# Optimization experiments

Hardware: AMD Instinct MI355X
Metric: run time of the kernel (lower is better)

Reference implementation:

```python
import jax, jax.numpy as jnp
import numpy as np

VOCAB = 32000
EMBED = 256
HIDDEN = 512
BATCH = 32
MAXLEN = 128


def setup_inputs() -> dict:
    key = jax.random.key(0)
    ks = jax.random.split(key, 8)
    s = 0.02
    return {
        "text": jax.random.randint(ks[0], (BATCH, MAXLEN), 0, VOCAB, dtype=jnp.int64),
        "embed": jax.random.normal(ks[1], (VOCAB, EMBED), dtype=jnp.float32) * s,
        "W_ih": jax.random.normal(ks[2], (4 * HIDDEN, EMBED), dtype=jnp.float32) * s,
        "W_hh": jax.random.normal(ks[3], (4 * HIDDEN, HIDDEN), dtype=jnp.float32) * s,
        "b_ih": jax.random.normal(ks[4], (4 * HIDDEN,), dtype=jnp.float32) * s,
        "b_hh": jax.random.normal(ks[5], (4 * HIDDEN,), dtype=jnp.float32) * s,
        "W_fc": jax.random.normal(ks[6], (VOCAB, HIDDEN), dtype=jnp.float32) * s,
        "b_fc": jax.random.normal(ks[7], (VOCAB,), dtype=jnp.float32) * s,
    }


def reference(text, embed, W_ih, W_hh, b_ih, b_hh, W_fc, b_fc):
    B, T = text.shape
    H = W_hh.shape[1]

    def step(carry, _):
        h, c, tok = carry
        x = embed[tok]                                  # [B, E] gather
        gates = x @ W_ih.T + b_ih + h @ W_hh.T + b_hh   # [B, 4H]
        i, f, g, o = jnp.split(gates, 4, axis=-1)       # PyTorch LSTMCell gate order
        i = jax.nn.sigmoid(i)
        f = jax.nn.sigmoid(f)
        g = jnp.tanh(g)
        o = jax.nn.sigmoid(o)
        c = f * c + i * g
        h = o * jnp.tanh(c)
        logits = h @ W_fc.T + b_fc                      # [B, V]
        tok = jnp.argmax(logits, axis=1)                # greedy feedback
        return (h, c, tok), logits

    # initial prediction = zeros[B,1] -> argmax = token 0; hidden=None -> zeros
    init = (
        jnp.zeros((B, H), dtype=embed.dtype),
        jnp.zeros((B, H), dtype=embed.dtype),
        jnp.zeros((B,), dtype=jnp.int32),
    )
    _, logits = jax.lax.scan(step, init, None, length=T)  # [T, B, V]
    return jnp.transpose(logits, (1, 0, 2))               # [B, T, V]
```

## Files before the change

kernel.cpp:

```cpp
#include <hip/hip_runtime.h>
#include <hip/hip_bf16.h>
#include <math.h>

#define VOCAB  32000
#define EMBED  256
#define HIDDEN 512
#define BATCH  32
#define MAXLEN 128
#define NCAND  250
#define VB     128

typedef __attribute__((ext_vector_type(8))) short bf16x8;
typedef __attribute__((ext_vector_type(8))) unsigned short ushort8;
typedef __attribute__((ext_vector_type(4))) float f32x4;

#define WS_C_OFF     0
#define WS_HHI_OFF   65536
#define WS_HLO_OFF   131072
#define WS_CAND_OFF  196608
#define WS_WHI_OFF   260608
#define WS_WLO_OFF   33028608
#define WS_ZERO_BYTES 196608

__device__ __forceinline__ unsigned int f32_ordered_key(float f) {
    unsigned int b = __float_as_uint(f);
    return (b & 0x80000000u) ? ~b : (b | 0x80000000u);
}
__device__ __forceinline__ unsigned short f2bf(float x) {
    __hip_bfloat16 h = __float2bfloat16(x);
    return *reinterpret_cast<unsigned short*>(&h);
}
__device__ __forceinline__ float bf2f(unsigned short u) {
    __hip_bfloat16 h = *reinterpret_cast<__hip_bfloat16*>(&u);
    return __bfloat162float(h);
}

__global__ __launch_bounds__(256) void split_w_kernel(
    const float* __restrict__ W, unsigned short* __restrict__ hi,
    unsigned short* __restrict__ lo, int n4)
{
    const int stride = gridDim.x * blockDim.x;
    for (int i = blockIdx.x * blockDim.x + threadIdx.x; i < n4; i += stride) {
        f32x4 w = ((const f32x4*)W)[i];
        ushort4 hv, lv;
        #pragma unroll
        for (int j = 0; j < 4; ++j) {
            float x = w[j];
            unsigned short hb = f2bf(x);
            ((unsigned short*)&hv)[j] = hb;
            ((unsigned short*)&lv)[j] = f2bf(x - bf2f(hb));
        }
        ((ushort4*)hi)[i] = hv;
        ((ushort4*)lo)[i] = lv;
    }
}

__global__ __launch_bounds__(256) void lstm_step_kernel(
    const float* __restrict__ embed,
    const float* __restrict__ W_ih, const float* __restrict__ W_hh,
    const float* __restrict__ b_ih, const float* __restrict__ b_hh,
    const unsigned long long* __restrict__ cand,
    const unsigned short* __restrict__ hhi_prev, const unsigned short* __restrict__ hlo_prev,
    unsigned short* __restrict__ hhi_next, unsigned short* __restrict__ hlo_next,
    float* __restrict__ c_buf, int t)
{
    __shared__ float x_t[EMBED][33];
    __shared__ float h_t[HIDDEN][33];
    __shared__ int   tok_s[BATCH];
    __shared__ unsigned long long credl[8][BATCH];
    __shared__ float part[2][4][BATCH][4];
    __shared__ float gate_s[2][4][BATCH];

    const int tid = threadIdx.x;

    if (t > 0) {
        const int rb = tid & 31, seg = tid >> 5;
        unsigned long long m = 0ull;
        for (int i = seg; i < NCAND; i += 8) {
            unsigned long long e = cand[(size_t)i * BATCH + rb];
            if (e > m) m = e;
        }
        credl[seg][rb] = m;
        __syncthreads();
        if (tid < BATCH) {
            unsigned long long mm = credl[0][tid];
            #pragma unroll
            for (int ss = 1; ss < 8; ++ss) if (credl[ss][tid] > mm) mm = credl[ss][tid];
            tok_s[tid] = (int)(~(unsigned int)(mm & 0xFFFFFFFFull));
        }
    } else {
        if (tid < BATCH) tok_s[tid] = 0;
    }
    __syncthreads();

    {
        const int sb = tid >> 3, slot = tid & 7;
        const float* er = embed + (size_t)tok_s[sb] * EMBED;
        #pragma unroll
        for (int i = 0; i < 8; ++i) {
            int e4 = i * 8 + slot;
            float4 v = ((const float4*)er)[e4];
            int e = e4 * 4;
            x_t[e + 0][sb] = v.x; x_t[e + 1][sb] = v.y;
            x_t[e + 2][sb] = v.z; x_t[e + 3][sb] = v.w;
        }
        const ushort8* hr = (const ushort8*)(hhi_prev + (size_t)sb * HIDDEN);
        const ushort8* lr = (const ushort8*)(hlo_prev + (size_t)sb * HIDDEN);
        #pragma unroll
        for (int i = 0; i < 8; ++i) {
            int u = i * 8 + slot;
            ushort8 hv = hr[u], lv = lr[u];
            #pragma unroll
            for (int e = 0; e < 8; ++e)
                h_t[u * 8 + e][sb] = bf2f((unsigned short)hv[e]) + bf2f((unsigned short)lv[e]);
        }
    }
    __syncthreads();

    const int b  = tid & 31;
    const int s  = (tid >> 5) & 3;
    const int jp = tid >> 7;
    const int j  = blockIdx.x * 2 + jp;

    float a0 = 0.f, a1 = 0.f, a2 = 0.f, a3 = 0.f;
    float d0 = 0.f, d1 = 0.f, d2 = 0.f, d3 = 0.f;

    {
        const float4* w0 = (const float4*)(W_ih + (size_t)j * EMBED) + s * 16;
        const float4* w1 = (const float4*)(W_ih + (size_t)(HIDDEN + j) * EMBED) + s * 16;
        const float4* w2 = (const float4*)(W_ih + (size_t)(2 * HIDDEN + j) * EMBED) + s * 16;
        const float4* w3 = (const float4*)(W_ih + (size_t)(3 * HIDDEN + j) * EMBED) + s * 16;
        #pragma unroll 4
        for (int g = 0; g < 16; ++g) {
            float4 W0 = w0[g], W1 = w1[g], W2 = w2[g], W3 = w3[g];
            int e = s * 64 + g * 4;
            float x0 = x_t[e + 0][b], x1 = x_t[e + 1][b], x2 = x_t[e + 2][b], x3 = x_t[e + 3][b];
            a0 = fmaf(W0.x, x0, a0); d0 = fmaf(W0.y, x1, d0); a0 = fmaf(W0.z, x2, a0); d0 = fmaf(W0.w, x3, d0);
            a1 = fmaf(W1.x, x0, a1); d1 = fmaf(W1.y, x1, d1); a1 = fmaf(W1.z, x2, a1); d1 = fmaf(W1.w, x3, d1);
            a2 = fmaf(W2.x, x0, a2); d2 = fmaf(W2.y, x1, d2); a2 = fmaf(W2.z, x2, a2); d2 = fmaf(W2.w, x3, d2);
            a3 = fmaf(W3.x, x0, a3); d3 = fmaf(W3.y, x1, d3); a3 = fmaf(W3.z, x2, a3); d3 = fmaf(W3.w, x3, d3);
        }
    }
    {
        const float4* w0 = (const float4*)(W_hh + (size_t)j * HIDDEN) + s * 32;
        const float4* w1 = (const float4*)(W_hh + (size_t)(HIDDEN + j) * HIDDEN) + s * 32;
        const float4* w2 = (const float4*)(W_hh + (size_t)(2 * HIDDEN + j) * HIDDEN) + s * 32;
        const float4* w3 = (const float4*)(W_hh + (size_t)(3 * HIDDEN + j) * HIDDEN) + s * 32;
        #pragma unroll 4
        for (int g = 0; g < 32; ++g) {
            float4 W0 = w0[g], W1 = w1[g], W2 = w2[g], W3 = w3[g];
            int k = s * 128 + g * 4;
            float x0 = h_t[k + 0][b], x1 = h_t[k + 1][b], x2 = h_t[k + 2][b], x3 = h_t[k + 3][b];
            a0 = fmaf(W0.x, x0, a0); d0 = fmaf(W0.y, x1, d0); a0 = fmaf(W0.z, x2, a0); d0 = fmaf(W0.w, x3, d0);
            a1 = fmaf(W1.x, x0, a1); d1 = fmaf(W1.y, x1, d1); a1 = fmaf(W1.z, x2, a1); d1 = fmaf(W1.w, x3, d1);
            a2 = fmaf(W2.x, x0, a2); d2 = fmaf(W2.y, x1, d2); a2 = fmaf(W2.z, x2, a2); d2 = fmaf(W2.w, x3, d2);
            a3 = fmaf(W3.x, x0, a3); d3 = fmaf(W3.y, x1, d3); a3 = fmaf(W3.z, x2, a3); d3 = fmaf(W3.w, x3, d3);
        }
    }
    part[jp][s][b][0] = a0 + d0;
    part[jp][s][b][1] = a1 + d1;
    part[jp][s][b][2] = a2 + d2;
    part[jp][s][b][3] = a3 + d3;
    __syncthreads();

    {
        const int gb = tid & 31, gate = (tid >> 5) & 3, gjp = tid >> 7;
        const int jj = blockIdx.x * 2 + gjp;
        float g = part[gjp][0][gb][gate] + part[gjp][1][gb][gate]
                + part[gjp][2][gb][gate] + part[gjp][3][gb][gate];
        g += b_ih[gate * HIDDEN + jj] + b_hh[gate * HIDDEN + jj];
        gate_s[gjp][gate][gb] = (gate == 2) ? tanhf(g) : 1.f / (1.f + expf(-g));
    }
    __syncthreads();

    if (tid < 64) {
        const int cb = tid & 31, cjp = tid >> 5;
        const int jj = blockIdx.x * 2 + cjp;
        const float iv = gate_s[cjp][0][cb], fv = gate_s[cjp][1][cb];
        const float gv = gate_s[cjp][2][cb], ov = gate_s[cjp][3][cb];
        const size_t off = (size_t)cb * HIDDEN + jj;
        float cn = fv * c_buf[off] + iv * gv;
        c_buf[off] = cn;
        float hv = ov * tanhf(cn);
        unsigned short hh = f2bf(hv);
        hhi_next[off] = hh;
        hlo_next[off] = f2bf(hv - bf2f(hh));
    }
}

#define MFMA(a, b, c) __builtin_amdgcn_mfma_f32_16x16x32_bf16((a), (b), (c), 0, 0, 0)
#define HPTR(arr, bb, cc) \
    ((const bf16x8*)((const char*)(arr) + ((((bb) * 1024) + (kg * 16) + (cc) * 64) ^ ((((bb) & 7)) << 4))))

__global__ __launch_bounds__(512) void logits_mfma_kernel(
    const unsigned short* __restrict__ Whi, const unsigned short* __restrict__ Wlo,
    const unsigned short* __restrict__ hhi, const unsigned short* __restrict__ hlo,
    const float* __restrict__ b_fc, float* __restrict__ out,
    unsigned long long* __restrict__ cand, int t)
{
    __shared__ unsigned short hs_hi[BATCH * HIDDEN];
    __shared__ unsigned short hs_lo[BATCH * HIDDEN];
    __shared__ unsigned long long red[8][BATCH];

    const int tid = threadIdx.x;

    const int w    = tid >> 6;
    const int lane = tid & 63;
    const int row  = lane & 15;
    const int kg   = lane >> 4;
    const int vwave = blockIdx.x * VB + w * 16;

    const unsigned short* wh = Whi + (size_t)(vwave + row) * HIDDEN + kg * 8;
    const unsigned short* wl = Wlo + (size_t)(vwave + row) * HIDDEN + kg * 8;

    bf16x8 whb[8], wlb[8];
    #pragma unroll
    for (int p = 0; p < 8; ++p) {
        whb[p] = *(const bf16x8*)(wh + p * 32);
        wlb[p] = *(const bf16x8*)(wl + p * 32);
    }

    #pragma unroll
    for (int i = 0; i < 8; ++i) {
        int u   = i * 512 + tid;
        int arr = u >> 11;
        int b   = (u >> 6) & 31;
        int k16 = u & 63;
        const unsigned short* src = (arr ? hlo : hhi) + (size_t)b * HIDDEN + k16 * 8;
        int4 v = *(const int4*)src;
        char* dst = (char*)(arr ? hs_lo : hs_hi) + ((b * 1024 + k16 * 16) ^ ((b & 7) << 4));
        *(int4*)dst = v;
    }
    __syncthreads();

    f32x4 acc0 = {0.f, 0.f, 0.f, 0.f};
    f32x4 acc1 = {0.f, 0.f, 0.f, 0.f};

    #pragma unroll
    for (int c = 0; c < 16; ++c) {
        bf16x8 cwh = whb[c & 7], cwl = wlb[c & 7];
        bf16x8 hh0 = *HPTR(hs_hi, row, c),      hh1 = *HPTR(hs_hi, row + 16, c);
        bf16x8 hl0 = *HPTR(hs_lo, row, c),      hl1 = *HPTR(hs_lo, row + 16, c);
        if (c + 8 < 16) {
            whb[c & 7] = *(const bf16x8*)(wh + (c + 8) * 32);
            wlb[c & 7] = *(const bf16x8*)(wl + (c + 8) * 32);
        }
        acc0 = MFMA(cwh, hh0, acc0); acc1 = MFMA(cwh, hh1, acc1);
        acc0 = MFMA(cwl, hh0, acc0); acc1 = MFMA(cwl, hh1, acc1);
        acc0 = MFMA(cwh, hl0, acc0); acc1 = MFMA(cwh, hl1, acc1);
    }

    const int v4 = vwave + kg * 4;
    f32x4 bias = *(const f32x4*)(b_fc + v4);
    f32x4 st0, st1;
    unsigned long long best0 = 0ull, best1 = 0ull;
    #pragma unroll
    for (int jj = 0; jj < 4; ++jj) {
        st0[jj] = acc0[jj] + bias[jj];
        st1[jj] = acc1[jj] + bias[jj];
        unsigned long long e0 = ((unsigned long long)f32_ordered_key(st0[jj]) << 32)
                              | (unsigned long long)(~(unsigned int)(v4 + jj));
        unsigned long long e1 = ((unsigned long long)f32_ordered_key(st1[jj]) << 32)
                              | (unsigned long long)(~(unsigned int)(v4 + jj));
        if (e0 > best0) best0 = e0;
        if (e1 > best1) best1 = e1;
    }
    __builtin_nontemporal_store(st0, (f32x4*)(out + ((size_t)row * MAXLEN + t) * VOCAB + v4));
    __builtin_nontemporal_store(st1, (f32x4*)(out + ((size_t)(row + 16) * MAXLEN + t) * VOCAB + v4));

    #pragma unroll
    for (int sft = 16; sft <= 32; sft <<= 1) {
        unsigned long long o0 = __shfl_xor(best0, sft, 64);
        unsigned long long o1 = __shfl_xor(best1, sft, 64);
        if (o0 > best0) best0 = o0;
        if (o1 > best1) best1 = o1;
    }
    if (kg == 0) { red[w][row] = best0; red[w][row + 16] = best1; }
    __syncthreads();
    if (tid < BATCH) {
        unsigned long long m = red[0][tid];
        #pragma unroll
        for (int ww = 1; ww < 8; ++ww) if (red[ww][tid] > m) m = red[ww][tid];
        cand[(size_t)blockIdx.x * BATCH + tid] = m;
    }
}

extern "C" void kernel_launch(void* const* d_in, const int* in_sizes, int n_in,
                              void* d_out, int out_size, void* d_ws, size_t ws_size,
                              hipStream_t stream) {
    const float* embed = (const float*)d_in[1];
    const float* W_ih  = (const float*)d_in[2];
    const float* W_hh  = (const float*)d_in[3];
    const float* b_ih  = (const float*)d_in[4];
    const float* b_hh  = (const float*)d_in[5];
    const float* W_fc  = (const float*)d_in[6];
    const float* b_fc  = (const float*)d_in[7];
    float* out = (float*)d_out;

    char* ws = (char*)d_ws;
    float* c_buf = (float*)(ws + WS_C_OFF);
    unsigned short* h_hi = (unsigned short*)(ws + WS_HHI_OFF);
    unsigned short* h_lo = (unsigned short*)(ws + WS_HLO_OFF);
    unsigned long long* cand = (unsigned long long*)(ws + WS_CAND_OFF);
    unsigned short* W_hi = (unsigned short*)(ws + WS_WHI_OFF);
    unsigned short* W_lo = (unsigned short*)(ws + WS_WLO_OFF);

    hipMemsetAsync(d_ws, 0, WS_ZERO_BYTES, stream);
    split_w_kernel<<<2048, 256, 0, stream>>>(W_fc, W_hi, W_lo, VOCAB * HIDDEN / 4);

    for (int t = 0; t < MAXLEN; ++t) {
        const int p = t & 1;
        unsigned short* hhi_prev = h_hi + (size_t)p * BATCH * HIDDEN;
        unsigned short* hlo_prev = h_lo + (size_t)p * BATCH * HIDDEN;
        unsigned short* hhi_next = h_hi + (size_t)(p ^ 1) * BATCH * HIDDEN;
        unsigned short* hlo_next = h_lo + (size_t)(p ^ 1) * BATCH * HIDDEN;
        lstm_step_kernel<<<256, 256, 0, stream>>>(
            embed, W_ih, W_hh, b_ih, b_hh, cand,
            hhi_prev, hlo_prev, hhi_next, hlo_next, c_buf, t);
        logits_mfma_kernel<<<NCAND, 512, 0, stream>>>(
            W_hi, W_lo, hhi_next, hlo_next, b_fc, out, cand, t);
    }
}
```

Baseline: 4.478 ms.

## Drop LDS staging in LSTM step; one hidden unit per block, 512 blocks

The LSTM step kernel no longer stages the embedding rows and hidden state into transposed shared-memory tiles. Each thread now reads its batch row's x and h slices straight from global memory into registers. Each block handles one hidden unit instead of two, with the K dimension split across 8 segments, and the grid doubles to 512 blocks. This removes the LDS fill, one barrier and per-block staging latency, and adds parallelism, at the cost of redundant global reads of x/h across blocks and uncoalesced per-thread row access.

```diff
diff --git a/kernel.cpp b/kernel.cpp
--- a/kernel.cpp
+++ b/kernel.cpp
@@ -64,14 +64,13 @@
     unsigned short* __restrict__ hhi_next, unsigned short* __restrict__ hlo_next,
     float* __restrict__ c_buf, int t)
 {
-    __shared__ float x_t[EMBED][33];
-    __shared__ float h_t[HIDDEN][33];
     __shared__ int   tok_s[BATCH];
     __shared__ unsigned long long credl[8][BATCH];
-    __shared__ float part[2][4][BATCH][4];
-    __shared__ float gate_s[2][4][BATCH];
+    __shared__ float part[8][4][BATCH];
+    __shared__ float gate_s[4][BATCH];
 
     const int tid = threadIdx.x;
+    const int j   = blockIdx.x;
 
     if (t > 0) {
         const int rb = tid & 31, seg = tid >> 5;
@@ -93,92 +92,74 @@
     }
     __syncthreads();
 
+    const int b = tid & 31;
+    const int s = tid >> 5;
+
+    float a0 = 0.f, a1 = 0.f, a2 = 0.f, a3 = 0.f;
+    float d0 = 0.f, d1 = 0.f, d2 = 0.f, d3 = 0.f;
+
     {
-        const int sb = tid >> 3, slot = tid & 7;
-        const float* er = embed + (size_t)tok_s[sb] * EMBED;
+        const float4* xr = (const float4*)(embed + (size_t)tok_s[b] * EMBED + s * 32);
+        const float4* w0 = (const float4*)(W_ih + (size_t)j * EMBED) + s * 8;
+        const float4* w1 = (const float4*)(W_ih + (size_t)(HIDDEN + j) * EMBED) + s * 8;
+        const float4* w2 = (const float4*)(W_ih + (size_t)(2 * HIDDEN + j) * EMBED) + s * 8;
+        const float4* w3 = (const float4*)(W_ih + (size_t)(3 * HIDDEN + j) * EMBED) + s * 8;
+        #pragma unroll
+        for (int g = 0; g < 8; ++g) {
+            float4 xv = xr[g];
+            float4 W0 = w0[g], W1 = w1[g], W2 = w2[g], W3 = w3[g];
+            a0 = fmaf(W0.x, xv.x, a0); d0 = fmaf(W0.y, xv.y, d0); a0 = fmaf(W0.z, xv.z, a0); d0 = fmaf(W0.w, xv.w, d0);
+            a1 = fmaf(W1.x, xv.x, a1); d1 = fmaf(W1.y, xv.y, d1); a1 = fmaf(W1.z, xv.z, a1); d1 = fmaf(W1.w, xv.w, d1);
+            a2 = fmaf(W2.x, xv.x, a2); d2 = fmaf(W2.y, xv.y, d2); a2 = fmaf(W2.z, xv.z, a2); d2 = fmaf(W2.w, xv.w, d2);
+            a3 = fmaf(W3.x, xv.x, a3); d3 = fmaf(W3.y, xv.y, d3); a3 = fmaf(W3.z, xv.z, a3); d3 = fmaf(W3.w, xv.w, d3);
+        }
+    }
+    {
+        const ushort8* hr = (const ushort8*)(hhi_prev + (size_t)b * HIDDEN + s * 64);
+        const ushort8* lr = (const ushort8*)(hlo_prev + (size_t)b * HIDDEN + s * 64);
+        const float4* w0 = (const float4*)(W_hh + (size_t)j * HIDDEN) + s * 16;
+        const float4* w1 = (const float4*)(W_hh + (size_t)(HIDDEN + j) * HIDDEN) + s * 16;
+        const float4* w2 = (const float4*)(W_hh + (size_t)(2 * HIDDEN + j) * HIDDEN) + s * 16;
+        const float4* w3 = (const float4*)(W_hh + (size_t)(3 * HIDDEN + j) * HIDDEN) + s * 16;
         #pragma unroll
         for (int i = 0; i < 8; ++i) {
-            int e4 = i * 8 + slot;
-            float4 v = ((const float4*)er)[e4];
-            int e = e4 * 4;
-            x_t[e + 0][sb] = v.x; x_t[e + 1][sb] = v.y;
-            x_t[e + 2][sb] = v.z; x_t[e + 3][sb] = v.w;
-        }
-        const ushort8* hr = (const ushort8*)(hhi_prev + (size_t)sb * HIDDEN);
-        const ushort8* lr = (const ushort8*)(hlo_prev + (size_t)sb * HIDDEN);
-        #pragma unroll
-        for (int i = 0; i < 8; ++i) {
-            int u = i * 8 + slot;
-            ushort8 hv = hr[u], lv = lr[u];
+            ushort8 hv = hr[i], lv = lr[i];
+            float hf[8];
             #pragma unroll
             for (int e = 0; e < 8; ++e)
-                h_t[u * 8 + e][sb] = bf2f((unsigned short)hv[e]) + bf2f((unsigned short)lv[e]);
-        }
-    }
-    __syncthreads();
-
-    const int b  = tid & 31;
-    const int s  = (tid >> 5) & 3;
-    const int jp = tid >> 7;
-    const int j  = blockIdx.x * 2 + jp;
-
-    float a0 = 0.f, a1 = 0.f, a2 = 0.f, a3 = 0.f;
-    float d0 = 0.f, d1 = 0.f, d2 = 0.f, d3 = 0.f;
-
-    {
-        const float4* w0 = (const float4*)(W_ih + (size_t)j * EMBED) + s * 16;
-        const float4* w1 = (const float4*)(W_ih + (size_t)(HIDDEN + j) * EMBED) + s * 16;
-        const float4* w2 = (const float4*)(W_ih + (size_t)(2 * HIDDEN + j) * EMBED) + s * 16;
-        const float4* w3 = (const float4*)(W_ih + (size_t)(3 * HIDDEN + j) * EMBED) + s * 16;
-        #pragma unroll 4
-        for (int g = 0; g < 16; ++g) {
-            float4 W0 = w0[g], W1 = w1[g], W2 = w2[g], W3 = w3[g];
-            int e = s * 64 + g * 4;
-            float x0 = x_t[e + 0][b], x1 = x_t[e + 1][b], x2 = x_t[e + 2][b], x3 = x_t[e + 3][b];
-            a0 = fmaf(W0.x, x0, a0); d0 = fmaf(W0.y, x1, d0); a0 = fmaf(W0.z, x2, a0); d0 = fmaf(W0.w, x3, d0);
-            a1 = fmaf(W1.x, x0, a1); d1 = fmaf(W1.y, x1, d1); a1 = fmaf(W1.z, x2, a1); d1 = fmaf(W1.w, x3, d1);
-            a2 = fmaf(W2.x, x0, a2); d2 = fmaf(W2.y, x1, d2); a2 = fmaf(W2.z, x2, a2); d2 = fmaf(W2.w, x3, d2);
-            a3 = fmaf(W3.x, x0, a3); d3 = fmaf(W3.y, x1, d3); a3 = fmaf(W3.z, x2, a3); d3 = fmaf(W3.w, x3, d3);
-        }
-    }
-    {
-        const float4* w0 = (const float4*)(W_hh + (size_t)j * HIDDEN) + s * 32;
-        const float4* w1 = (const float4*)(W_hh + (size_t)(HIDDEN + j) * HIDDEN) + s * 32;
-        const float4* w2 = (const float4*)(W_hh + (size_t)(2 * HIDDEN + j) * HIDDEN) + s * 32;
-        const float4* w3 = (const float4*)(W_hh + (size_t)(3 * HIDDEN + j) * HIDDEN) + s * 32;
-        #pragma unroll 4
-        for (int g = 0; g < 32; ++g) {
-            float4 W0 = w0[g], W1 = w1[g], W2 = w2[g], W3 = w3[g];
-            int k = s * 128 + g * 4;
-            float x0 = h_t[k + 0][b], x1 = h_t[k + 1][b], x2 = h_t[k + 2][b], x3 = h_t[k + 3][b];
-            a0 = fmaf(W0.x, x0, a0); d0 = fmaf(W0.y, x1, d0); a0 = fmaf(W0.z, x2, a0); d0 = fmaf(W0.w, x3, d0);
-            a1 = fmaf(W1.x, x0, a1); d1 = fmaf(W1.y, x1, d1); a1 = fmaf(W1.z, x2, a1); d1 = fmaf(W1.w, x3, d1);
-            a2 = fmaf(W2.x, x0, a2); d2 = fmaf(W2.y, x1, d2); a2 = fmaf(W2.z, x2, a2); d2 = fmaf(W2.w, x3, d2);
-            a3 = fmaf(W3.x, x0, a3); d3 = fmaf(W3.y, x1, d3); a3 = fmaf(W3.z, x2, a3); d3 = fmaf(W3.w, x3, d3);
-        }
-    }
-    part[jp][s][b][0] = a0 + d0;
-    part[jp][s][b][1] = a1 + d1;
-    part[jp][s][b][2] = a2 + d2;
-    part[jp][s][b][3] = a3 + d3;
-    __syncthreads();
-
-    {
-        const int gb = tid & 31, gate = (tid >> 5) & 3, gjp = tid >> 7;
-        const int jj = blockIdx.x * 2 + gjp;
-        float g = part[gjp][0][gb][gate] + part[gjp][1][gb][gate]
-                + part[gjp][2][gb][gate] + part[gjp][3][gb][gate];
-        g += b_ih[gate * HIDDEN + jj] + b_hh[gate * HIDDEN + jj];
-        gate_s[gjp][gate][gb] = (gate == 2) ? tanhf(g) : 1.f / (1.f + expf(-g));
-    }
-    __syncthreads();
-
-    if (tid < 64) {
-        const int cb = tid & 31, cjp = tid >> 5;
-        const int jj = blockIdx.x * 2 + cjp;
-        const float iv = gate_s[cjp][0][cb], fv = gate_s[cjp][1][cb];
-        const float gv = gate_s[cjp][2][cb], ov = gate_s[cjp][3][cb];
-        const size_t off = (size_t)cb * HIDDEN + jj;
+                hf[e] = bf2f((unsigned short)hv[e]) + bf2f((unsigned short)lv[e]);
+            #pragma unroll
+            for (int q = 0; q < 2; ++q) {
+                float4 W0 = w0[i * 2 + q], W1 = w1[i * 2 + q], W2 = w2[i * 2 + q], W3 = w3[i * 2 + q];
+                float x0 = hf[q * 4 + 0], x1 = hf[q * 4 + 1], x2 = hf[q * 4 + 2], x3 = hf[q * 4 + 3];
+                a0 = fmaf(W0.x, x0, a0); d0 = fmaf(W0.y, x1, d0); a0 = fmaf(W0.z, x2, a0); d0 = fmaf(W0.w, x3, d0);
+                a1 = fmaf(W1.x, x0, a1); d1 = fmaf(W1.y, x1, d1); a1 = fmaf(W1.z, x2, a1); d1 = fmaf(W1.w, x3, d1);
+                a2 = fmaf(W2.x, x0, a2); d2 = fmaf(W2.y, x1, d2); a2 = fmaf(W2.z, x2, a2); d2 = fmaf(W2.w, x3, d2);
+                a3 = fmaf(W3.x, x0, a3); d3 = fmaf(W3.y, x1, d3); a3 = fmaf(W3.z, x2, a3); d3 = fmaf(W3.w, x3, d3);
+            }
+        }
+    }
+    part[s][0][b] = a0 + d0;
+    part[s][1][b] = a1 + d1;
+    part[s][2][b] = a2 + d2;
+    part[s][3][b] = a3 + d3;
+    __syncthreads();
+
+    if (tid < 128) {
+        const int gb = tid & 31, gate = tid >> 5;
+        float g = 0.f;
+        #pragma unroll
+        for (int ss = 0; ss < 8; ++ss) g += part[ss][gate][gb];
+        g += b_ih[gate * HIDDEN + j] + b_hh[gate * HIDDEN + j];
+        gate_s[gate][gb] = (gate == 2) ? tanhf(g) : 1.f / (1.f + expf(-g));
+    }
+    __syncthreads();
+
+    if (tid < 32) {
+        const int cb = tid;
+        const float iv = gate_s[0][cb], fv = gate_s[1][cb];
+        const float gv = gate_s[2][cb], ov = gate_s[3][cb];
+        const size_t off = (size_t)cb * HIDDEN + j;
         float cn = fv * c_buf[off] + iv * gv;
         c_buf[off] = cn;
         float hv = ov * tanhf(cn);
@@ -314,7 +295,7 @@
         unsigned short* hlo_prev = h_lo + (size_t)p * BATCH * HIDDEN;
         unsigned short* hhi_next = h_hi + (size_t)(p ^ 1) * BATCH * HIDDEN;
         unsigned short* hlo_next = h_lo + (size_t)(p ^ 1) * BATCH * HIDDEN;
-        lstm_step_kernel<<<256, 256, 0, stream>>>(
+        lstm_step_kernel<<<512, 256, 0, stream>>>(
             embed, W_ih, W_hh, b_ih, b_hh, cand,
             hhi_prev, hlo_prev, hhi_next, hlo_next, c_buf, t);
         logits_mfma_kernel<<<NCAND, 512, 0, stream>>>(
```

Result: slower. 4.704 ms (+5.1%).
